# Performance work log

Measured on AMD Instinct MI355X. Metric: run time of the kernel, lower is better.

## Reference

```python
import jax, jax.numpy as jnp
import numpy as np

B, IN, OUT, D = 8192, 1024, 1024, 4
STEPS = 8
DT = 1.0
EPS = 1e-12  # matches torch F.normalize default eps


def _normalize(v):
    # L2-normalize along last dim, torch-style: v / max(||v||, eps)
    n = jnp.sqrt(jnp.sum(v * v, axis=-1, keepdims=True))
    return v / jnp.maximum(n, EPS)


def setup_inputs() -> dict:
    key = jax.random.key(0)
    k_x, k_w, k_c = jax.random.split(key, 3)
    x = jax.random.normal(k_x, (B, IN), dtype=jnp.float32)
    W_in = jax.random.normal(k_w, (IN, OUT, D), dtype=jnp.float32) * 0.2
    omega = jnp.zeros((OUT, D), dtype=jnp.float32)
    coupling = jax.random.normal(k_c, (OUT, OUT), dtype=jnp.float32)  # coupling_scale = 1.0
    return {"x": x, "W_in": W_in, "omega": omega, "coupling": coupling}


def reference(x, W_in, omega, coupling):
    # v: [B, OUT, D]
    v = jnp.einsum('bi,iod->bod', x, W_in)
    v = _normalize(v)
    K = jnp.tanh(coupling)  # [OUT, OUT]

    def step(v, _):
        agg = jnp.einsum('ij,bjd->bid', K, v)
        v = _normalize(v + DT * (agg + omega))
        return v, None

    v, _ = jax.lax.scan(step, v, None, length=STEPS)
    return v
```

## Files before the change

### kernel.cpp

```cpp
#include <hip/hip_runtime.h>
#include <math.h>


#define B_SZ   8192
#define OUT_SZ 1024
#define STEPS  8
#define PLANE  ((size_t)B_SZ * OUT_SZ)
#define WPLANE ((size_t)OUT_SZ * OUT_SZ)

typedef __attribute__((ext_vector_type(8))) short  short8;
typedef __attribute__((ext_vector_type(4))) float  f32x4;
typedef unsigned short us;

__device__ __forceinline__ us f2bf(float f) {
    union { float f; unsigned u; } v; v.f = f;
    unsigned r = v.u + 0x7FFFu + ((v.u >> 16) & 1u);
    return (us)(r >> 16);
}
__device__ __forceinline__ float bf2f(us h) {
    union { unsigned u; float f; } v; v.u = ((unsigned)h) << 16;
    return v.f;
}
__device__ __forceinline__ void dma16(const void* g, void* l) {
    __builtin_amdgcn_global_load_lds(
        (const __attribute__((address_space(1))) void*)g,
        (__attribute__((address_space(3))) void*)l, 16, 0, 0);
}
__device__ __forceinline__ float rnorm4(float a, float b, float c, float d) {
    float n2 = a * a + b * b + c * c + d * d;
    float s = rsqrtf(fmaxf(n2, 1e-24f));
    return s * (1.5f - 0.5f * n2 * s * s);
}

__global__ void tanhsplit_kernel(const float* __restrict__ c,
                                 us* __restrict__ Khi, us* __restrict__ Klo) {
    int idx = blockIdx.x * 256 + threadIdx.x;
    float val = tanhf(c[idx]) + (((idx >> 10) == (idx & (OUT_SZ - 1))) ? 1.0f : 0.0f);
    us hi = f2bf(val);
    Khi[idx] = hi;
    Klo[idx] = f2bf(val - bf2f(hi));
}

__global__ void xsplit_kernel(const float* __restrict__ x,
                              us* __restrict__ Xhi, us* __restrict__ Xlo) {
    int idx = (blockIdx.x * 256 + threadIdx.x) * 4;
    float4 v = *(const float4*)&x[idx];
    float p[4] = { v.x, v.y, v.z, v.w };
    unsigned h01, h23, l01, l23;
    us h[4], l[4];
#pragma unroll
    for (int t = 0; t < 4; ++t) {
        h[t] = f2bf(p[t]);
        l[t] = f2bf(p[t] - bf2f(h[t]));
    }
    h01 = (unsigned)h[0] | ((unsigned)h[1] << 16);
    h23 = (unsigned)h[2] | ((unsigned)h[3] << 16);
    l01 = (unsigned)l[0] | ((unsigned)l[1] << 16);
    l23 = (unsigned)l[2] | ((unsigned)l[3] << 16);
    ((unsigned*)Xhi)[idx / 2]     = h01;
    ((unsigned*)Xhi)[idx / 2 + 1] = h23;
    ((unsigned*)Xlo)[idx / 2]     = l01;
    ((unsigned*)Xlo)[idx / 2 + 1] = l23;
}

__global__ void wprep_kernel(const float* __restrict__ W,
                             us* __restrict__ Wthi, us* __restrict__ Wtlo) {
    int idx = blockIdx.x * 256 + threadIdx.x;
    int d  = idx & 3;
    int o  = (idx >> 2) & (OUT_SZ - 1);
    int kc = idx >> 12;
    us h[16], l[16];
#pragma unroll
    for (int t = 0; t < 16; ++t) {
        float v = W[((size_t)(kc * 16 + t) * OUT_SZ + o) * 4 + d];
        h[t] = f2bf(v);
        l[t] = f2bf(v - bf2f(h[t]));
    }
    size_t base = (size_t)d * WPLANE + (size_t)o * OUT_SZ + kc * 16;
#pragma unroll
    for (int t = 0; t < 16; ++t) { Wthi[base + t] = h[t]; Wtlo[base + t] = l[t]; }
}

__device__ __forceinline__ void wait_vm8() {
    asm volatile("s_waitcnt vmcnt(8)" ::: "memory");
    __builtin_amdgcn_sched_barrier(0);
}
__device__ __forceinline__ void wait_vm0() {
    asm volatile("s_waitcnt vmcnt(0)" ::: "memory");
    __builtin_amdgcn_sched_barrier(0);
}
__device__ __forceinline__ void wait_lgkm0() {
    asm volatile("s_waitcnt lgkmcnt(0)" ::: "memory");
    __builtin_amdgcn_sched_barrier(0);
}

__global__ __launch_bounds__(512, 2) void step_mfma_kernel(
    const us* __restrict__ Vhi, const us* __restrict__ Vlo,
    const us* __restrict__ Khi, const us* __restrict__ Klo,
    const float* __restrict__ omega,
    us* __restrict__ Ohi, us* __restrict__ Olo,
    float* __restrict__ out, int final_step)
{
    __shared__ short As[2][16384];
    __shared__ short Bs[2][16384];

    const int tid = threadIdx.x;
    const int ln = tid & 63, wv = tid >> 6;
    const int wm = wv & 1, wn = wv >> 1;

    const int lid = blockIdx.y * 4 + blockIdx.x;
    const int n   = (lid & 7) * 64 + (lid >> 3);
    const int i0 = (n & 3) * 256;
    const int b0 = (n >> 2) * 64;

    const us* gsrc[8];
    short*    ldst[8];
#pragma unroll
    for (int j = 0; j < 8; ++j) {
        int t = wv * 8 + j;
        if (t < 32) {
            int d = t >> 3, bg = (t >> 1) & 3, hl = t & 1;
            int b = b0 + bg * 16 + (ln & 15);
            const us* base = hl ? Vlo : Vhi;
            gsrc[j] = base + (size_t)d * PLANE + (size_t)b * OUT_SZ + (ln >> 4) * 8;
            ldst[j] = &As[0][((d * 4 + bg) * 2 + hl) * 512];
        } else {
            int u = t - 32, ig = u >> 1, hl = u & 1;
            int i = i0 + ig * 16 + (ln & 15);
            const us* base = hl ? Klo : Khi;
            gsrc[j] = base + (size_t)i * OUT_SZ + (ln >> 4) * 8;
            ldst[j] = &Bs[0][(ig * 2 + hl) * 512];
        }
    }

    f32x4 acc[4][2][4];
#pragma unroll
    for (int d = 0; d < 4; ++d)
#pragma unroll
        for (int bh = 0; bh < 2; ++bh)
#pragma unroll
            for (int nf = 0; nf < 4; ++nf) acc[d][bh][nf] = (f32x4){0.f, 0.f, 0.f, 0.f};

#pragma unroll
    for (int j = 0; j < 8; ++j) { dma16(gsrc[j], ldst[j]); gsrc[j] += 32; }
#pragma unroll
    for (int j = 0; j < 8; ++j) { dma16(gsrc[j], ldst[j] + 16384); gsrc[j] += 32; }

    int cur = 0;
    for (int it = 0; it < 32; ++it) {
        if (it < 31) wait_vm8(); else wait_vm0();
        __builtin_amdgcn_s_barrier();

        short8 bfr[4][2];
#pragma unroll
        for (int nf = 0; nf < 4; ++nf)
#pragma unroll
            for (int hl = 0; hl < 2; ++hl)
                bfr[nf][hl] = *(const short8*)&Bs[cur][((wn * 4 + nf) * 2 + hl) * 512 + ln * 8];

#pragma unroll
        for (int bh = 0; bh < 2; ++bh) {
            const int bg = wm * 2 + bh;
            short8 afr[4][2];
#pragma unroll
            for (int d = 0; d < 4; ++d)
#pragma unroll
                for (int hl = 0; hl < 2; ++hl)
                    afr[d][hl] = *(const short8*)&As[cur][((d * 4 + bg) * 2 + hl) * 512 + ln * 8];

            __builtin_amdgcn_s_setprio(1);
#pragma unroll
            for (int d = 0; d < 4; ++d)
#pragma unroll
                for (int nf = 0; nf < 4; ++nf)
                    acc[d][bh][nf] = __builtin_amdgcn_mfma_f32_16x16x32_bf16(afr[d][0], bfr[nf][0], acc[d][bh][nf], 0, 0, 0);
#pragma unroll
            for (int d = 0; d < 4; ++d)
#pragma unroll
                for (int nf = 0; nf < 4; ++nf)
                    acc[d][bh][nf] = __builtin_amdgcn_mfma_f32_16x16x32_bf16(afr[d][1], bfr[nf][0], acc[d][bh][nf], 0, 0, 0);
#pragma unroll
            for (int d = 0; d < 4; ++d)
#pragma unroll
                for (int nf = 0; nf < 4; ++nf)
                    acc[d][bh][nf] = __builtin_amdgcn_mfma_f32_16x16x32_bf16(afr[d][0], bfr[nf][1], acc[d][bh][nf], 0, 0, 0);
            __builtin_amdgcn_s_setprio(0);
        }

        wait_lgkm0();
        __builtin_amdgcn_s_barrier();
        if (it + 2 < 32) {
#pragma unroll
            for (int j = 0; j < 8; ++j) {
                dma16(gsrc[j], ldst[j] + cur * 16384);
                gsrc[j] += 32;
            }
        }
        cur ^= 1;
    }

#pragma unroll
    for (int bh = 0; bh < 2; ++bh)
#pragma unroll
        for (int nf = 0; nf < 4; ++nf) {
            const int i = i0 + wn * 64 + nf * 16 + (ln & 15);
            const f32x4 om = *(const f32x4*)&omega[i * 4];
#pragma unroll
            for (int reg = 0; reg < 4; ++reg) {
                const int b = b0 + wm * 32 + bh * 16 + (ln >> 4) * 4 + reg;
                float tv[4];
#pragma unroll
                for (int d = 0; d < 4; ++d) tv[d] = acc[d][bh][nf][reg] + om[d];
                float s = rnorm4(tv[0], tv[1], tv[2], tv[3]);
                if (final_step) {
                    f32x4 rr = { tv[0] * s, tv[1] * s, tv[2] * s, tv[3] * s };
                    *(f32x4*)&out[((size_t)b * OUT_SZ + i) * 4] = rr;
                } else {
#pragma unroll
                    for (int d = 0; d < 4; ++d) {
                        float val = tv[d] * s;
                        us hi = f2bf(val);
                        size_t idx = (size_t)d * PLANE + (size_t)b * OUT_SZ + i;
                        Ohi[idx] = hi;
                        Olo[idx] = f2bf(val - bf2f(hi));
                    }
                }
            }
        }
}

__global__ __launch_bounds__(512, 2) void init_mfma_kernel(
    const us* __restrict__ Xhi, const us* __restrict__ Xlo,
    const us* __restrict__ Wthi, const us* __restrict__ Wtlo,
    us* __restrict__ Ohi, us* __restrict__ Olo)
{
    __shared__ short As[2][16384];
    __shared__ short Bs[2][16384];

    const int tid = threadIdx.x;
    const int ln = tid & 63, wv = tid >> 6;
    const int wm = wv & 3, wn = wv >> 2;

    const int lid = blockIdx.y * 16 + blockIdx.x;
    const int n   = (lid & 7) * 64 + (lid >> 3);
    const int o0 = ((n >> 2) & 15) * 64;
    const int b0 = ((n & 3) + ((n >> 6) << 2)) * 256;

    const us* gsrc[8];
    short*    ldst[8];
#pragma unroll
    for (int j = 0; j < 8; ++j) {
        int t = wv * 8 + j;
        if (t < 32) {
            int bg = t >> 1, hl = t & 1;
            int b = b0 + bg * 16 + (ln & 15);
            const us* base = hl ? Xlo : Xhi;
            gsrc[j] = base + (size_t)b * 1024 + (ln >> 4) * 8;
            ldst[j] = &As[0][(bg * 2 + hl) * 512];
        } else {
            int u = t - 32, d = u >> 3, og = (u >> 1) & 3, hl = u & 1;
            int o = o0 + og * 16 + (ln & 15);
            const us* base = hl ? Wtlo : Wthi;
            gsrc[j] = base + (size_t)d * WPLANE + (size_t)o * OUT_SZ + (ln >> 4) * 8;
            ldst[j] = &Bs[0][((d * 4 + og) * 2 + hl) * 512];
        }
    }

    f32x4 acc[4][4][2];
#pragma unroll
    for (int d = 0; d < 4; ++d)
#pragma unroll
        for (int mf = 0; mf < 4; ++mf)
#pragma unroll
            for (int nf = 0; nf < 2; ++nf) acc[d][mf][nf] = (f32x4){0.f, 0.f, 0.f, 0.f};

#pragma unroll
    for (int j = 0; j < 8; ++j) { dma16(gsrc[j], ldst[j]); gsrc[j] += 32; }
#pragma unroll
    for (int j = 0; j < 8; ++j) { dma16(gsrc[j], ldst[j] + 16384); gsrc[j] += 32; }

    int cur = 0;
    for (int it = 0; it < 32; ++it) {
        if (it < 31) wait_vm8(); else wait_vm0();
        __builtin_amdgcn_s_barrier();

        short8 bfr[4][2][2];
#pragma unroll
        for (int d = 0; d < 4; ++d)
#pragma unroll
            for (int nf = 0; nf < 2; ++nf)
#pragma unroll
                for (int hl = 0; hl < 2; ++hl)
                    bfr[d][nf][hl] = *(const short8*)&Bs[cur][((d * 4 + (wn * 2 + nf)) * 2 + hl) * 512 + ln * 8];

#pragma unroll
        for (int mf = 0; mf < 4; ++mf) {
            const int bg = wm * 4 + mf;
            short8 afr[2];
#pragma unroll
            for (int hl = 0; hl < 2; ++hl)
                afr[hl] = *(const short8*)&As[cur][(bg * 2 + hl) * 512 + ln * 8];

            __builtin_amdgcn_s_setprio(1);
#pragma unroll
            for (int d = 0; d < 4; ++d)
#pragma unroll
                for (int nf = 0; nf < 2; ++nf)
                    acc[d][mf][nf] = __builtin_amdgcn_mfma_f32_16x16x32_bf16(afr[0], bfr[d][nf][0], acc[d][mf][nf], 0, 0, 0);
#pragma unroll
            for (int d = 0; d < 4; ++d)
#pragma unroll
                for (int nf = 0; nf < 2; ++nf)
                    acc[d][mf][nf] = __builtin_amdgcn_mfma_f32_16x16x32_bf16(afr[1], bfr[d][nf][0], acc[d][mf][nf], 0, 0, 0);
#pragma unroll
            for (int d = 0; d < 4; ++d)
#pragma unroll
                for (int nf = 0; nf < 2; ++nf)
                    acc[d][mf][nf] = __builtin_amdgcn_mfma_f32_16x16x32_bf16(afr[0], bfr[d][nf][1], acc[d][mf][nf], 0, 0, 0);
            __builtin_amdgcn_s_setprio(0);
        }

        wait_lgkm0();
        __builtin_amdgcn_s_barrier();
        if (it + 2 < 32) {
#pragma unroll
            for (int j = 0; j < 8; ++j) {
                dma16(gsrc[j], ldst[j] + cur * 16384);
                gsrc[j] += 32;
            }
        }
        cur ^= 1;
    }

#pragma unroll
    for (int mf = 0; mf < 4; ++mf)
#pragma unroll
        for (int nf = 0; nf < 2; ++nf) {
            const int o = o0 + (wn * 2 + nf) * 16 + (ln & 15);
#pragma unroll
            for (int reg = 0; reg < 4; ++reg) {
                const int b = b0 + (wm * 4 + mf) * 16 + (ln >> 4) * 4 + reg;
                float tv[4];
#pragma unroll
                for (int d = 0; d < 4; ++d) tv[d] = acc[d][mf][nf][reg];
                float s = rnorm4(tv[0], tv[1], tv[2], tv[3]);
#pragma unroll
                for (int d = 0; d < 4; ++d) {
                    float val = tv[d] * s;
                    us hi = f2bf(val);
                    size_t idx = (size_t)d * PLANE + (size_t)b * OUT_SZ + o;
                    Ohi[idx] = hi;
                    Olo[idx] = f2bf(val - bf2f(hi));
                }
            }
        }
}

extern "C" void kernel_launch(void* const* d_in, const int* in_sizes, int n_in,
                              void* d_out, int out_size, void* d_ws, size_t ws_size,
                              hipStream_t stream) {
    const float* x        = (const float*)d_in[0];
    const float* W_in     = (const float*)d_in[1];
    const float* omega    = (const float*)d_in[2];
    const float* coupling = (const float*)d_in[3];
    float* out = (float*)d_out;

    us* Khi = (us*)d_ws;
    us* Klo = Khi + WPLANE;
    us* Ahi = Klo + WPLANE;
    us* Alo = Ahi + 4 * PLANE;
    us* Bhi = (us*)d_out;
    us* Blo = Bhi + 4 * PLANE;

    us* Xhi  = Ahi;
    us* Xlo  = Xhi + (size_t)B_SZ * 1024;
    us* Wthi = Xlo + (size_t)B_SZ * 1024;
    us* Wtlo = Wthi + 4 * WPLANE;

    tanhsplit_kernel<<<(OUT_SZ * OUT_SZ) / 256, 256, 0, stream>>>(coupling, Khi, Klo);
    xsplit_kernel<<<(B_SZ * 1024) / 1024, 256, 0, stream>>>(x, Xhi, Xlo);
    wprep_kernel<<<(4 * OUT_SZ * 64) / 256, 256, 0, stream>>>(W_in, Wthi, Wtlo);

    init_mfma_kernel<<<dim3(OUT_SZ / 64, B_SZ / 256), 512, 0, stream>>>(
        Xhi, Xlo, Wthi, Wtlo, Bhi, Blo);

    for (int s = 0; s < STEPS; ++s) {
        const us* Shi = (s & 1) ? Ahi : Bhi;
        const us* Slo = (s & 1) ? Alo : Blo;
        us*       Dhi = (s & 1) ? Bhi : Ahi;
        us*       Dlo = (s & 1) ? Blo : Alo;
        int fin = (s == STEPS - 1);
        step_mfma_kernel<<<dim3(OUT_SZ / 256, B_SZ / 64), 512, 0, stream>>>(
            Shi, Slo, Khi, Klo, omega, Dhi, Dlo, out, fin);
    }
}
```

Baseline: 2.265 ms.

## Remap block-to-tile order for L2 locality and restructure init MFMA fragment loads

Changes the mapping of workgroup IDs to output tiles in both the step and init kernels. The new bit-interleaved order groups neighbouring blocks on each XCD so they share operand tiles in L2. In the init kernel, the inner loop now iterates over d outermost, loading B fragments per d and all A fragments up front, which changes LDS read scheduling and register pressure. The epilogues are reordered to loop over rows before columns, and omega is hoisted before the epilogue loop. Possible risks are higher register use and different store coalescing.

New measurement: 2.084 ms. -8.0%, faster.

```diff
diff --git a/kernel.cpp b/kernel.cpp
--- a/kernel.cpp
+++ b/kernel.cpp
@@ -109,9 +109,11 @@
     const int wm = wv & 1, wn = wv >> 1;
 
     const int lid = blockIdx.y * 4 + blockIdx.x;
-    const int n   = (lid & 7) * 64 + (lid >> 3);
-    const int i0 = (n & 3) * 256;
-    const int b0 = (n >> 2) * 64;
+    const int X   = lid & 7, nn = lid >> 3;
+    const int i_idx = (nn & 1) | (((nn >> 2) & 1) << 1);
+    const int b_idx = ((nn >> 1) & 1) | (((nn >> 3) & 1) << 1) | (((nn >> 4) & 3) << 2);
+    const int i0 = i_idx * 256;
+    const int b0 = (X * 16 + b_idx) * 64;
 
     const us* gsrc[8];
     short*    ldst[8];
@@ -199,18 +201,22 @@
         cur ^= 1;
     }
 
+    f32x4 om[4];
+#pragma unroll
+    for (int nf = 0; nf < 4; ++nf)
+        om[nf] = *(const f32x4*)&omega[(i0 + wn * 64 + nf * 16 + (ln & 15)) * 4];
+
 #pragma unroll
     for (int bh = 0; bh < 2; ++bh)
 #pragma unroll
-        for (int nf = 0; nf < 4; ++nf) {
-            const int i = i0 + wn * 64 + nf * 16 + (ln & 15);
-            const f32x4 om = *(const f32x4*)&omega[i * 4];
-#pragma unroll
-            for (int reg = 0; reg < 4; ++reg) {
-                const int b = b0 + wm * 32 + bh * 16 + (ln >> 4) * 4 + reg;
+        for (int reg = 0; reg < 4; ++reg) {
+            const int b = b0 + wm * 32 + bh * 16 + (ln >> 4) * 4 + reg;
+#pragma unroll
+            for (int nf = 0; nf < 4; ++nf) {
+                const int i = i0 + wn * 64 + nf * 16 + (ln & 15);
                 float tv[4];
 #pragma unroll
-                for (int d = 0; d < 4; ++d) tv[d] = acc[d][bh][nf][reg] + om[d];
+                for (int d = 0; d < 4; ++d) tv[d] = acc[d][bh][nf][reg] + om[nf][d];
                 float s = rnorm4(tv[0], tv[1], tv[2], tv[3]);
                 if (final_step) {
                     f32x4 rr = { tv[0] * s, tv[1] * s, tv[2] * s, tv[3] * s };
@@ -242,9 +248,11 @@
     const int wm = wv & 3, wn = wv >> 2;
 
     const int lid = blockIdx.y * 16 + blockIdx.x;
-    const int n   = (lid & 7) * 64 + (lid >> 3);
-    const int o0 = ((n >> 2) & 15) * 64;
-    const int b0 = ((n & 3) + ((n >> 6) << 2)) * 256;
+    const int X   = lid & 7, nn = lid >> 3;
+    const int o_idx = (nn & 1) | (((nn >> 2) & 1) << 1) | (((nn >> 4) & 3) << 2);
+    const int b_idx = ((nn >> 1) & 1) | (((nn >> 3) & 1) << 1);
+    const int o0 = o_idx * 64;
+    const int b0 = (X * 4 + b_idx) * 256;
 
     const us* gsrc[8];
     short*    ldst[8];
@@ -284,39 +292,37 @@
         if (it < 31) wait_vm8(); else wait_vm0();
         __builtin_amdgcn_s_barrier();
 
-        short8 bfr[4][2][2];
-#pragma unroll
-        for (int d = 0; d < 4; ++d)
+#pragma unroll
+        for (int d = 0; d < 4; ++d) {
+            short8 bfr[2][2];
 #pragma unroll
             for (int nf = 0; nf < 2; ++nf)
 #pragma unroll
                 for (int hl = 0; hl < 2; ++hl)
-                    bfr[d][nf][hl] = *(const short8*)&Bs[cur][((d * 4 + (wn * 2 + nf)) * 2 + hl) * 512 + ln * 8];
-
-#pragma unroll
-        for (int mf = 0; mf < 4; ++mf) {
-            const int bg = wm * 4 + mf;
-            short8 afr[2];
-#pragma unroll
-            for (int hl = 0; hl < 2; ++hl)
-                afr[hl] = *(const short8*)&As[cur][(bg * 2 + hl) * 512 + ln * 8];
+                    bfr[nf][hl] = *(const short8*)&Bs[cur][((d * 4 + (wn * 2 + nf)) * 2 + hl) * 512 + ln * 8];
+            short8 afr[4][2];
+#pragma unroll
+            for (int mf = 0; mf < 4; ++mf)
+#pragma unroll
+                for (int hl = 0; hl < 2; ++hl)
+                    afr[mf][hl] = *(const short8*)&As[cur][((wm * 4 + mf) * 2 + hl) * 512 + ln * 8];
 
             __builtin_amdgcn_s_setprio(1);
 #pragma unroll
-            for (int d = 0; d < 4; ++d)
+            for (int mf = 0; mf < 4; ++mf)
 #pragma unroll
                 for (int nf = 0; nf < 2; ++nf)
-                    acc[d][mf][nf] = __builtin_amdgcn_mfma_f32_16x16x32_bf16(afr[0], bfr[d][nf][0], acc[d][mf][nf], 0, 0, 0);
-#pragma unroll
-            for (int d = 0; d < 4; ++d)
+                    acc[d][mf][nf] = __builtin_amdgcn_mfma_f32_16x16x32_bf16(afr[mf][0], bfr[nf][0], acc[d][mf][nf], 0, 0, 0);
+#pragma unroll
+            for (int mf = 0; mf < 4; ++mf)
 #pragma unroll
                 for (int nf = 0; nf < 2; ++nf)
-                    acc[d][mf][nf] = __builtin_amdgcn_mfma_f32_16x16x32_bf16(afr[1], bfr[d][nf][0], acc[d][mf][nf], 0, 0, 0);
-#pragma unroll
-            for (int d = 0; d < 4; ++d)
+                    acc[d][mf][nf] = __builtin_amdgcn_mfma_f32_16x16x32_bf16(afr[mf][1], bfr[nf][0], acc[d][mf][nf], 0, 0, 0);
+#pragma unroll
+            for (int mf = 0; mf < 4; ++mf)
 #pragma unroll
                 for (int nf = 0; nf < 2; ++nf)
-                    acc[d][mf][nf] = __builtin_amdgcn_mfma_f32_16x16x32_bf16(afr[0], bfr[d][nf][1], acc[d][mf][nf], 0, 0, 0);
+                    acc[d][mf][nf] = __builtin_amdgcn_mfma_f32_16x16x32_bf16(afr[mf][0], bfr[nf][1], acc[d][mf][nf], 0, 0, 0);
             __builtin_amdgcn_s_setprio(0);
         }
 
@@ -335,11 +341,11 @@
 #pragma unroll
     for (int mf = 0; mf < 4; ++mf)
 #pragma unroll
-        for (int nf = 0; nf < 2; ++nf) {
-            const int o = o0 + (wn * 2 + nf) * 16 + (ln & 15);
-#pragma unroll
-            for (int reg = 0; reg < 4; ++reg) {
-                const int b = b0 + (wm * 4 + mf) * 16 + (ln >> 4) * 4 + reg;
+        for (int reg = 0; reg < 4; ++reg) {
+            const int b = b0 + (wm * 4 + mf) * 16 + (ln >> 4) * 4 + reg;
+#pragma unroll
+            for (int nf = 0; nf < 2; ++nf) {
+                const int o = o0 + (wn * 2 + nf) * 16 + (ln & 15);
                 float tv[4];
 #pragma unroll
                 for (int d = 0; d < 4; ++d) tv[d] = acc[d][mf][nf][reg];
```
